# Kernel optimization log

Hardware: AMD Instinct MI355X
Metric: run time of the kernel (lower is better)

## Reference

```python
import jax, jax.numpy as jnp
import numpy as np

B = 128          # graphs
N = 512          # nodes per graph
NT = B * N       # total nodes = 65536
E = NT * 16      # total edges = 1048576
IN = 64
H = 128
OUT = 2
L = 4            # num_layers
RATIO = 0.8


def setup_inputs() -> dict:
    key = jax.random.key(0)
    ks = jax.random.split(key, 20)

    def w(k, shape, fan_in):
        return jax.random.normal(k, shape, jnp.float32) / np.sqrt(fan_in)

    x = jax.random.normal(ks[0], (NT, IN), jnp.float32)
    edge_index = jax.random.randint(ks[1], (2, E), 0, NT, dtype=jnp.int32)
    batch = (jnp.arange(NT) // N).astype(jnp.int32)  # equal-size graphs

    return {
        "x": x,
        "edge_index": edge_index,
        "batch": batch,
        # conv1: GraphConv(IN, H, aggr='mean') -> lin_rel (w/ bias) + lin_root (no bias)
        "W1_rel": w(ks[2], (IN, H), IN),
        "W1_root": w(ks[3], (IN, H), IN),
        "b1": jnp.zeros((H,), jnp.float32),
        # convs[0..2]: GraphConv(H, H, aggr='mean'), stacked
        "Wc_rel": w(ks[4], (L - 1, H, H), H),
        "Wc_root": w(ks[5], (L - 1, H, H), H),
        "bc": jnp.zeros((L - 1, H), jnp.float32),
        # SAGPooling score GNN: GraphConv(H, 1) with default aggr='add'
        "pw_rel": w(ks[6], (H,), H),
        "pw_root": w(ks[7], (H,), H),
        "pb": jnp.zeros((1,), jnp.float32),
        # MLP head
        "lin1_W": w(ks[8], (L * H, H), L * H),
        "lin1_b": jnp.zeros((H,), jnp.float32),
        "lin2_W": w(ks[9], (H, OUT), H),
        "lin2_b": jnp.zeros((OUT,), jnp.float32),
    }


def _graph_conv_mean(x, src, dst, emask, W_rel, W_root, b, n):
    # PyG GraphConv: lin_rel(mean_{j->i} x_j) + lin_root(x_i); masked edges excluded.
    msg = x[src] * emask[:, None]                                  # [E, D] gather
    s = jax.ops.segment_sum(msg, dst, num_segments=n)              # [n, D] scatter-add
    cnt = jax.ops.segment_sum(emask, dst, num_segments=n)          # [n]
    agg = s / jnp.maximum(cnt, 1.0)[:, None]                       # zero for isolated nodes
    return agg @ W_rel + x @ W_root + b


def reference(x, edge_index, batch, W1_rel, W1_root, b1, Wc_rel, Wc_root, bc,
              pw_rel, pw_root, pb, lin1_W, lin1_b, lin2_W, lin2_b):
    src = edge_index[0]
    dst = edge_index[1]
    emask = jnp.ones((E,), jnp.float32)
    n = NT
    npg = N  # nodes per graph (all graphs equal size)

    h = jax.nn.relu(_graph_conv_mean(x, src, dst, emask, W1_rel, W1_root, b1, n))
    xs = [h.reshape(B, npg, H).mean(axis=1)]  # global_mean_pool

    for i in range(L - 1):
        h = jax.nn.relu(_graph_conv_mean(h, src, dst, emask, Wc_rel[i], Wc_root[i], bc[i], n))
        xs.append(h.reshape(B, npg, H).mean(axis=1))
        if i % 2 == 0 and i < L - 2:
            # ---- SAGPooling: score via GraphConv(H,1) with add aggregation ----
            smsg = jax.ops.segment_sum(h[src] * emask[:, None], dst, num_segments=n)
            score = smsg @ pw_rel + h @ pw_root + pb[0]            # [n]
            k = int(np.ceil(RATIO * npg))
            topv, topi = jax.lax.top_k(score.reshape(B, npg), k)   # per-graph top-k
            perm = (jnp.arange(B)[:, None] * npg + topi).reshape(-1)  # global kept ids
            h = h[perm] * jnp.tanh(topv.reshape(-1))[:, None]
            # remap edges; edges touching dropped nodes get masked out
            node_map = jnp.full((n,), -1, jnp.int32).at[perm].set(
                jnp.arange(B * k, dtype=jnp.int32))
            ns, nd = node_map[src], node_map[dst]
            keep = ((ns >= 0) & (nd >= 0)).astype(jnp.float32)
            emask = emask * keep
            src = jnp.where(ns >= 0, ns, 0)
            dst = jnp.where(nd >= 0, nd, 0)
            n = B * k
            npg = k

    xcat = jnp.concatenate(xs, axis=-1)                            # JumpingKnowledge 'cat'
    out = jax.nn.relu(xcat @ lin1_W + lin1_b)
    # dropout is identity in eval mode
    out = out @ lin2_W + lin2_b
    return jax.nn.log_softmax(out, axis=-1)
```

## Files before the change

kernel.cpp:

```cpp
#include <hip/hip_runtime.h>
#include <math.h>

#define NT 65536
#define EE 1048576
#define NB 128
#define KK 410
#define HH 128

typedef short bf16x8 __attribute__((ext_vector_type(8)));
typedef float f32x4 __attribute__((ext_vector_type(4)));
typedef unsigned int u32x4 __attribute__((ext_vector_type(4)));

__device__ __align__(16) unsigned short g_xb[(size_t)NT * 64];
__device__ __align__(16) unsigned short g_hb1[(size_t)NT * HH];
__device__ __align__(16) unsigned short g_hb2[(size_t)NT * HH];
__device__ __align__(16) unsigned short g_wt1[128 * 128];
__device__ __align__(16) unsigned short g_wtc[3 * 128 * 256];
__device__ __align__(16) unsigned short g_xbs[(size_t)8 * NT * 8];
__device__ __align__(16) unsigned short g_hbs[(size_t)8 * NT * 16];
__device__ __align__(16) unsigned short g_agg[(size_t)16 * NT * 8];
__device__ unsigned short g_csr1u[EE];
__device__ unsigned short g_keptu[NT];
__device__ unsigned int g_ebuck[EE];
__device__ int g_bcnt[128];
__device__ int g_bbase[129];
__device__ int g_bcur[128];
__device__ float g_trel[NT];
__device__ float g_troot[NT];
__device__ float g_gatef[NT];
__device__ float g_kinv[NT];
__device__ float g_xc4[4 * NB * 4 * 128];
__device__ int g_rows1[NT + 1];

__device__ __forceinline__ unsigned short* ubuf(int id) {
    switch (id) {
        case 0: return g_xb;
        case 1: return g_hb1;
        case 2: return g_hb2;
        case 3: return g_wt1;
        case 4: return g_wtc;
    }
    return g_xb;
}

__device__ __forceinline__ float b2f(unsigned short u) {
    union { unsigned int i; float f; } v;
    v.i = ((unsigned int)u) << 16;
    return v.f;
}
__device__ __forceinline__ unsigned short f2b(float f) {
    unsigned int x = __float_as_uint(f);
    unsigned int r = x + 0x7fffu + ((x >> 16) & 1u);
    return (unsigned short)(r >> 16);
}
__device__ __forceinline__ unsigned int pk2(float a, float b) {
    return (unsigned int)f2b(a) | ((unsigned int)f2b(b) << 16);
}
__device__ __forceinline__ unsigned int mul2(unsigned int wd, float g) {
    float lo = b2f((unsigned short)(wd & 0xffffu)) * g;
    float hi = b2f((unsigned short)(wd >> 16)) * g;
    return pk2(lo, hi);
}
__device__ __forceinline__ bf16x8 scale8(bf16x8 a, float g) {
    bf16x8 r;
#pragma unroll
    for (int i = 0; i < 8; i++) {
        unsigned short u = (unsigned short)a[i];
        r[i] = (short)f2b(b2f(u) * g);
    }
    return r;
}

__global__ void k_prep(const float* __restrict__ x,
                       const float* __restrict__ W1r, const float* __restrict__ W1o,
                       const float* __restrict__ Wcr, const float* __restrict__ Wco) {
    int tid = blockIdx.x * 256 + threadIdx.x;
    if (tid < 1048576) {
        float4 v = *(const float4*)&x[(size_t)tid * 4];
        unsigned int lo = pk2(v.x, v.y);
        unsigned int hi = pk2(v.z, v.w);
        *(uint2*)&g_xb[(size_t)tid * 4] = make_uint2(lo, hi);
        int node = tid >> 4;
        int sl = (tid & 15) >> 1;
        int of = (tid & 1) * 4;
        *(uint2*)&g_xbs[(((size_t)sl) * NT + node) * 8 + of] = make_uint2(lo, hi);
    } else if (tid < 1048576 + 16384) {
        int r = tid - 1048576;
        int k = r & 127, n = r >> 7;
        float v = (k < 64) ? W1r[k * 128 + n] : W1o[(k - 64) * 128 + n];
        g_wt1[n * 128 + k] = f2b(v);
    } else if (tid < 1048576 + 16384 + 98304) {
        int r = tid - (1048576 + 16384);
        int l = r >> 15;
        int k = r & 255, n = (r >> 8) & 127;
        float v = (k < 128) ? Wcr[l * 16384 + k * 128 + n]
                            : Wco[l * 16384 + (k - 128) * 128 + n];
        g_wtc[l * 32768 + n * 256 + k] = f2b(v);
    } else if (tid < 1048576 + 16384 + 98304 + 128) {
        g_bcnt[tid - (1048576 + 16384 + 98304)] = 0;
    }
}

__global__ __launch_bounds__(256) void k_bhist(const int* __restrict__ dst) {
    __shared__ int h[128];
    if (threadIdx.x < 128) h[threadIdx.x] = 0;
    __syncthreads();
    int e0 = (blockIdx.x * 256 + threadIdx.x) * 4;
    int4 d = *(const int4*)&dst[e0];
    atomicAdd(&h[d.x >> 9], 1);
    atomicAdd(&h[d.y >> 9], 1);
    atomicAdd(&h[d.z >> 9], 1);
    atomicAdd(&h[d.w >> 9], 1);
    __syncthreads();
    if (threadIdx.x < 128 && h[threadIdx.x]) atomicAdd(&g_bcnt[threadIdx.x], h[threadIdx.x]);
}

__global__ __launch_bounds__(128) void k_bscan() {
    __shared__ int s[128];
    int t = threadIdx.x;
    int v = g_bcnt[t];
    s[t] = v;
    __syncthreads();
    for (int off = 1; off < 128; off <<= 1) {
        int u = (t >= off) ? s[t - off] : 0;
        __syncthreads();
        s[t] += u;
        __syncthreads();
    }
    g_bbase[t] = s[t] - v;
    g_bcur[t] = s[t] - v;
    if (t == 127) g_bbase[128] = s[127];
}

__global__ __launch_bounds__(256) void k_bscatter(const int* __restrict__ src,
// ... 14 lines not shown
    if (threadIdx.x < 128) {
        int c = h[threadIdx.x];
        base[threadIdx.x] = c ? atomicAdd(&g_bcur[threadIdx.x], c) : 0;
        h[threadIdx.x] = 0;
    }
    __syncthreads();
    int r0 = atomicAdd(&h[b0], 1);
    g_ebuck[base[b0] + r0] = ((unsigned int)(d.x & 511) << 16) | (unsigned int)s.x;
    int r1 = atomicAdd(&h[b1], 1);
    g_ebuck[base[b1] + r1] = ((unsigned int)(d.y & 511) << 16) | (unsigned int)s.y;
    int r2 = atomicAdd(&h[b2], 1);
    g_ebuck[base[b2] + r2] = ((unsigned int)(d.z & 511) << 16) | (unsigned int)s.z;
    int r3 = atomicAdd(&h[b3], 1);
    g_ebuck[base[b3] + r3] = ((unsigned int)(d.w & 511) << 16) | (unsigned int)s.w;
}

__global__ __launch_bounds__(512) void k_bcsr() {
    __shared__ int hist[512];
    __shared__ int offs[512];
    __shared__ int cur[512];
    int g = blockIdx.x, t = threadIdx.x;
    hist[t] = 0;
    cur[t] = 0;
    __syncthreads();
    int b0 = g_bbase[g], b1 = g_bbase[g + 1];
    for (int e = b0 + t; e < b1; e += 512) {
        unsigned int p = g_ebuck[e];
        atomicAdd(&hist[p >> 16], 1);
    }
    __syncthreads();
    int v = hist[t];
    offs[t] = v;
    __syncthreads();
    for (int off = 1; off < 512; off <<= 1) {
        int u = (t >= off) ? offs[t - off] : 0;
        __syncthreads();
        offs[t] += u;
        __syncthreads();
    }
    int excl = offs[t] - v;
    g_rows1[g * 512 + t] = b0 + excl;
    if (t == 511) g_rows1[g * 512 + 512] = b0 + excl + v;
    __syncthreads();
    offs[t] = excl;
    __syncthreads();
    for (int e = b0 + t; e < b1; e += 512) {
        unsigned int p = g_ebuck[e];
        int dl = p >> 16;
        int r = atomicAdd(&cur[dl], 1);
        g_csr1u[b0 + offs[dl] + r] = (unsigned short)(p & 0xFFFFu);
    }
}

#define ACCP(wd, J) { acc[J] += b2f((unsigned short)((wd) & 0xffffu)); acc[(J) + 1] += b2f((unsigned short)((wd) >> 16)); }
#define ACCQ(q, B) ACCP(q.x, B) ACCP(q.y, (B) + 2) ACCP(q.z, (B) + 4) ACCP(q.w, (B) + 6)

template <int F, int DEN>
__global__ __launch_bounds__(256) void k_agg(int srcId) {
    const unsigned short* src = (srcId == 0) ? g_xbs : g_hbs;
    int s = blockIdx.x & 7;
    int node = (blockIdx.x >> 3) * 256 + threadIdx.x;
    const unsigned short* sp = src + (size_t)s * NT * F;
    int r0 = g_rows1[node], r1 = g_rows1[node + 1];
    float inv;
    if (DEN) {
        inv = g_kinv[node];
    } else {
        int c = r1 - r0;
        inv = 1.0f / (float)(c > 0 ? c : 1);
    }
    float acc[F];
#pragma unroll
    for (int i = 0; i < F; i++) acc[i] = 0.f;
    int e = r0;
    for (; e + 2 <= r1; e += 2) {
        int i0 = g_csr1u[e], i1 = g_csr1u[e + 1];
        if constexpr (F == 16) {
            uint4 a0 = *(const uint4*)&sp[(size_t)i0 * 16];
            uint4 a1 = *(const uint4*)&sp[(size_t)i0 * 16 + 8];
            uint4 b0 = *(const uint4*)&sp[(size_t)i1 * 16];
            uint4 b1 = *(const uint4*)&sp[(size_t)i1 * 16 + 8];
            ACCQ(a0, 0) ACCQ(a1, 8) ACCQ(b0, 0) ACCQ(b1, 8)
        } else {
            uint4 a0 = *(const uint4*)&sp[(size_t)i0 * 8];
            uint4 b0 = *(const uint4*)&sp[(size_t)i1 * 8];
            ACCQ(a0, 0) ACCQ(b0, 0)
        }
    }
    for (; e < r1; e++) {
        int i0 = g_csr1u[e];
        if constexpr (F == 16) {
            uint4 a0 = *(const uint4*)&sp[(size_t)i0 * 16];
            uint4 a1 = *(const uint4*)&sp[(size_t)i0 * 16 + 8];
            ACCQ(a0, 0) ACCQ(a1, 8)
        } else {
            uint4 a0 = *(const uint4*)&sp[(size_t)i0 * 8];
            ACCQ(a0, 0)
        }
    }
    int gb = (F == 16) ? (2 * s) : s;
    u32x4 o;
    o[0] = pk2(acc[0] * inv, acc[1] * inv);
    o[1] = pk2(acc[2] * inv, acc[3] * inv);
    o[2] = pk2(acc[4] * inv, acc[5] * inv);
    o[3] = pk2(acc[6] * inv, acc[7] * inv);
    __builtin_nontemporal_store(o, (u32x4*)&g_agg[((size_t)gb * NT + node) * 8]);
    if constexpr (F == 16) {
        u32x4 o2;
        o2[0] = pk2(acc[8] * inv, acc[9] * inv);
        o2[1] = pk2(acc[10] * inv, acc[11] * inv);
        o2[2] = pk2(acc[12] * inv, acc[13] * inv);
        o2[3] = pk2(acc[14] * inv, acc[15] * inv);
        __builtin_nontemporal_store(o2, (u32x4*)&g_agg[((size_t)(2 * s + 1) * NT + node) * 8]);
    }
}

__global__ __launch_bounds__(256) void k_kinv() {
    int node = blockIdx.x * 256 + threadIdx.x;
    int r0 = g_rows1[node], r1 = g_rows1[node + 1];
    int kc = 0;
    for (int e = r0; e < r1; e++) kc += (int)g_keptu[g_csr1u[e]];
    g_kinv[node] = 1.0f / (float)(kc > 0 ? kc : 1);
}

__global__ __launch_bounds__(256) void k_gateS() {
    int tid = blockIdx.x * 256 + threadIdx.x;
    int n = tid >> 3, s = tid & 7;
    float g = g_gatef[n];
    const unsigned short* srcp = &g_hb2[(size_t)n * 128 + s * 16];
    uint4 a = *(const uint4*)srcp;
    uint4 b = *(const uint4*)(srcp + 8);
    uint4 oa, ob;
    oa.x = mul2(a.x, g); oa.y = mul2(a.y, g); oa.z = mul2(a.z, g); oa.w = mul2(a.w, g);
    ob.x = mul2(b.x, g); ob.y = mul2(b.y, g); ob.z = mul2(b.z, g); ob.w = mul2(b.w, g);
    unsigned short* d = &g_hbs[((size_t)s * NT + n) * 16];
    *(uint4*)d = oa;
    *(uint4*)(d + 8) = ob;
}

template <int KA, int KB, int MASKED, int DOTS, int BGATE, int WSL>
__global__ __launch_bounds__(256) void k_mm(int bId, int wId, int wOfs,
                                            const float* __restrict__ bias, int outId, int sec,
                                            const float* __restrict__ pwr,
                                            const float* __restrict__ pwt) {
    __shared__ float s[128];
    const unsigned short* Bp = ubuf(bId);
    const unsigned short* Wt = ubuf(wId) + wOfs;
    unsigned short* out = ubuf(outId);
    int rowbase = blockIdx.x * 128;
    const int K = KA + KB;
    int lane = threadIdx.x & 63;
    int w = threadIdx.x >> 6;
    int n16 = lane & 15, quad = lane >> 4;
    int rowloc = w * 32;
    int rowg = rowbase + rowloc;
    int g = blockIdx.x >> 2, qb = blockIdx.x & 3;
    float ga0 = BGATE ? g_gatef[rowg + n16] : 1.0f;
    float ga1 = BGATE ? g_gatef[rowg + 16 + n16] : 1.0f;
    f32x4 acc[2][8];
#pragma unroll
    for (int rt = 0; rt < 2; rt++)
#pragma unroll
        for (int ct = 0; ct < 8; ct++)
#pragma unroll
            for (int i = 0; i < 4; i++) acc[rt][ct][i] = 0.f;

#pragma unroll
    for (int ks = 0; ks < K / 32; ks++) {
        int k0 = ks * 32;
        bf16x8 a0, a1;
        if (k0 < KA) {
            int fg = (k0 + quad * 8) >> 3;
            a0 = *(const bf16x8*)&g_agg[((size_t)fg * NT + rowg + n16) * 8];
            a1 = *(const bf16x8*)&g_agg[((size_t)fg * NT + rowg + 16 + n16) * 8];
        } else {
            int kk = k0 - KA;
            a0 = *(const bf16x8*)&Bp[(size_t)(rowg + n16) * KB + kk + quad * 8];
            a1 = *(const bf16x8*)&Bp[(size_t)(rowg + 16 + n16) * KB + kk + quad * 8];
            if (BGATE) { a0 = scale8(a0, ga0); a1 = scale8(a1, ga1); }
        }
#pragma unroll
        for (int ct = 0; ct < 8; ct++) {
            bf16x8 b = *(const bf16x8*)&Wt[(size_t)(ct * 16 + n16) * K + k0 + quad * 8];
            acc[0][ct] = __builtin_amdgcn_mfma_f32_16x16x32_bf16(a0, b, acc[0][ct], 0, 0, 0);
            acc[1][ct] = __builtin_amdgcn_mfma_f32_16x16x32_bf16(a1, b, acc[1][ct], 0, 0, 0);
        }
    }

    if (threadIdx.x < 128) s[threadIdx.x] = 0.f;
#pragma unroll
    for (int rt = 0; rt < 2; rt++) {
        float m[4];
#pragma unroll
        for (int i = 0; i < 4; i++) {
            int r = rowg + rt * 16 + quad * 4 + i;
            m[i] = (!MASKED || g_keptu[r]) ? 1.0f : 0.0f;
        }
#pragma unroll
        for (int ct = 0; ct < 8; ct++) {
            int c = ct * 16 + n16;
            float bv = bias[c];
#pragma unroll
            for (int i = 0; i < 4; i++) {
                int r = rowg + rt * 16 + quad * 4 + i;
                float v = fmaxf(acc[rt][ct][i] + bv, 0.f) * m[i];
                acc[rt][ct][i] = v;
                unsigned short hv = f2b(v);
                out[(size_t)r * 128 + c] = hv;
                if (WSL) g_hbs[((size_t)(c >> 4) * NT + r) * 16 + (c & 15)] = hv;
            }
        }
    }
    __syncthreads();

#pragma unroll
    for (int ct = 0; ct < 8; ct++) {
        float p = 0.f;
#pragma unroll
        for (int rt = 0; rt < 2; rt++)
#pragma unroll
            for (int i = 0; i < 4; i++) p += acc[rt][ct][i];
        p += __shfl_xor(p, 16);
        p += __shfl_xor(p, 32);
        if (quad == 0) atomicAdd(&s[ct * 16 + n16], p);
    }

    if (DOTS) {
        float pr[8], pt[8];
#pragma unroll
        for (int ct = 0; ct < 8; ct++) {
            pr[ct] = pwr[ct * 16 + n16];
            pt[ct] = pwt[ct * 16 + n16];
        }
#pragma unroll
        for (int rt = 0; rt < 2; rt++)
#pragma unroll
            for (int i = 0; i < 4; i++) {
                float dr = 0.f, dt = 0.f;
#pragma unroll
                for (int ct = 0; ct < 8; ct++) {
                    dr += acc[rt][ct][i] * pr[ct];
                    dt += acc[rt][ct][i] * pt[ct];
                }
                dr += __shfl_xor(dr, 1); dt += __shfl_xor(dt, 1);
                dr += __shfl_xor(dr, 2); dt += __shfl_xor(dt, 2);
                dr += __shfl_xor(dr, 4); dt += __shfl_xor(dt, 4);
                dr += __shfl_xor(dr, 8); dt += __shfl_xor(dt, 8);
                if (n16 == 0) {
                    int r = rowg + rt * 16 + quad * 4 + i;
                    g_trel[r] = dr;
                    g_troot[r] = dt;
                }
            }
    }
    __syncthreads();
    if (threadIdx.x < 128)
        g_xc4[((sec * NB + g) * 4 + qb) * 128 + threadIdx.x] = s[threadIdx.x];
}

__global__ __launch_bounds__(256) void k_topk(const float* __restrict__ pb) {
    __shared__ float sv[512];
    __shared__ int si[512];
    int g = blockIdx.x, t = threadIdx.x;
    float pbv = pb[0];
    for (int l = t; l < 512; l += 256) {
        int node = g * 512 + l;
        int r0 = g_rows1[node], r1 = g_rows1[node + 1];
        float s = 0.f;
        int e = r0;
        for (; e + 4 <= r1; e += 4) {
            float s0 = g_trel[g_csr1u[e]];
            float s1 = g_trel[g_csr1u[e + 1]];
            float s2 = g_trel[g_csr1u[e + 2]];
            float s3 = g_trel[g_csr1u[e + 3]];
            s += (s0 + s1) + (s2 + s3);
        }
        for (; e < r1; e++) s += g_trel[g_csr1u[e]];
        sv[l] = s + g_troot[node] + pbv;
        si[l] = l;
    }
    __syncthreads();
    for (int k = 2; k <= 512; k <<= 1) {
        for (int j = k >> 1; j > 0; j >>= 1) {
            for (int i = t; i < 512; i += 256) {
                int p = i ^ j;
                if (p > i) {
                    float va = sv[i], vb = sv[p];
                    int ia = si[i], ib = si[p];
                    bool aFirst = (va > vb) || (va == vb && ia < ib);
                    bool up = ((i & k) == 0);
                    if (up != aFirst) { sv[i] = vb; sv[p] = va; si[i] = ib; si[p] = ia; }
                }
            }
            __syncthreads();
        }
    }
    for (int r = t; r < 512; r += 256) {
        int old = g * 512 + si[r];
        if (r < KK) {
            g_gatef[old] = tanhf(sv[r]);
            g_keptu[old] = 1;
        } else {
            g_gatef[old] = 0.f;
            g_keptu[old] = 0;
        }
    }
}

__global__ __launch_bounds__(128) void k_head(const float* __restrict__ W1, const float* __restrict__ b1,
                                              const float* __restrict__ W2, const float* __restrict__ b2,
// ... 6 lines not shown
        const float* p = &g_xc4[((sec * NB + g) * 4) * 128 + c];
        float v = p[0] + p[128] + p[256] + p[384];
        float inv = (sec < 2) ? (1.0f / 512.0f) : (1.0f / 410.0f);
        xr[i] = v * inv;
    }
    __syncthreads();
    float acc = b1[t];
    for (int k = 0; k < 512; k++) acc += xr[k] * W1[k * 128 + t];
    acc = fmaxf(acc, 0.f);
    r0[t] = acc * W2[t * 2 + 0];
    r1[t] = acc * W2[t * 2 + 1];
    __syncthreads();
    for (int off = 64; off > 0; off >>= 1) {
        if (t < off) { r0[t] += r0[t + off]; r1[t] += r1[t + off]; }
        __syncthreads();
    }
    if (t == 0) {
        float z0 = r0[0] + b2[0], z1 = r1[0] + b2[1];
        float m = fmaxf(z0, z1);
        float l = m + logf(expf(z0 - m) + expf(z1 - m));
        out[g * 2 + 0] = z0 - l;
        out[g * 2 + 1] = z1 - l;
    }
}

extern "C" void kernel_launch(void* const* d_in, const int* in_sizes, int n_in,
                              void* d_out, int out_size, void* d_ws, size_t ws_size,
                              hipStream_t stream) {
    const float* x = (const float*)d_in[0];
    const int* ei = (const int*)d_in[1];
    const int* src = ei;
    const int* dst = ei + EE;
    const float* W1r = (const float*)d_in[3];
    const float* W1o = (const float*)d_in[4];
    const float* b1 = (const float*)d_in[5];
    const float* Wcr = (const float*)d_in[6];
    const float* Wco = (const float*)d_in[7];
    const float* bc = (const float*)d_in[8];
    const float* pwr = (const float*)d_in[9];
    const float* pwt = (const float*)d_in[10];
    const float* pb = (const float*)d_in[11];
    const float* l1W = (const float*)d_in[12];
    const float* l1b = (const float*)d_in[13];
    const float* l2W = (const float*)d_in[14];
    const float* l2b = (const float*)d_in[15];
    float* out = (float*)d_out;

    k_prep<<<(1048576 + 16384 + 98304 + 128 + 255) / 256, 256, 0, stream>>>(x, W1r, W1o, Wcr, Wco);

    k_bhist<<<1024, 256, 0, stream>>>(dst);
    k_bscan<<<1, 128, 0, stream>>>();
    k_bscatter<<<1024, 256, 0, stream>>>(src, dst);
    k_bcsr<<<128, 512, 0, stream>>>();

    k_agg<8, 0><<<2048, 256, 0, stream>>>(0);
    k_mm<64, 64, 0, 0, 0, 1><<<512, 256, 0, stream>>>(0, 3, 0, b1, 1, 0, pwr, pwt);

    k_agg<16, 0><<<2048, 256, 0, stream>>>(1);
    k_mm<128, 128, 0, 1, 0, 0><<<512, 256, 0, stream>>>(1, 4, 0, bc, 2, 1, pwr, pwt);

    k_topk<<<NB, 256, 0, stream>>>(pb);
    k_kinv<<<NT / 256, 256, 0, stream>>>();
    k_gateS<<<2048, 256, 0, stream>>>();

    k_agg<16, 1><<<2048, 256, 0, stream>>>(1);
    k_mm<128, 128, 1, 0, 1, 1><<<512, 256, 0, stream>>>(2, 4, 32768, bc + 128, 1, 2, pwr, pwt);

    k_agg<16, 1><<<2048, 256, 0, stream>>>(1);
    k_mm<128, 128, 1, 0, 0, 0><<<512, 256, 0, stream>>>(1, 4, 65536, bc + 256, 2, 3, pwr, pwt);

    k_head<<<NB, 128, 0, stream>>>(l1W, l1b, l2W, l2b, out);
}
```

Measured before the change: 529.3 us.

## Degree-sort aggregation nodes, store activations sliced, gather last layer in 8-bit

Adds a per-graph node permutation sorted by in-degree so each aggregation wavefront processes nodes of similar edge counts, which reduces loop divergence. CSR neighbour indices are now read four at a time. Layer activations are written only in the feature-sliced layout through a shared-memory transpose, and the matmul root operand reads that layout, which removes the extra row-major copy. The last layer's neighbour gather reads a custom 8-bit float encoding (values clamped at 496) instead of bf16, halving the gather bytes at the cost of extra precision loss.

```diff
diff --git a/kernel.cpp b/kernel.cpp
--- a/kernel.cpp
+++ b/kernel.cpp
@@ -11,20 +11,21 @@
 typedef float f32x4 __attribute__((ext_vector_type(4)));
 typedef unsigned int u32x4 __attribute__((ext_vector_type(4)));
 
-__device__ __align__(16) unsigned short g_xb[(size_t)NT * 64];
-__device__ __align__(16) unsigned short g_hb1[(size_t)NT * HH];
+__device__ __align__(16) unsigned short g_xbs[(size_t)8 * NT * 8];
+__device__ __align__(16) unsigned short g_hs1[(size_t)8 * NT * 16];
+__device__ __align__(16) unsigned short g_hgs[(size_t)8 * NT * 16];
 __device__ __align__(16) unsigned short g_hb2[(size_t)NT * HH];
+__device__ __align__(16) unsigned char  g_h8b[(size_t)8 * NT * 16];
+__device__ __align__(16) unsigned short g_agg[(size_t)16 * NT * 8];
 __device__ __align__(16) unsigned short g_wt1[128 * 128];
 __device__ __align__(16) unsigned short g_wtc[3 * 128 * 256];
-__device__ __align__(16) unsigned short g_xbs[(size_t)8 * NT * 8];
-__device__ __align__(16) unsigned short g_hbs[(size_t)8 * NT * 16];
-__device__ __align__(16) unsigned short g_agg[(size_t)16 * NT * 8];
-__device__ unsigned short g_csr1u[EE];
+__device__ __align__(16) unsigned short g_csr1u[EE];
 __device__ unsigned short g_keptu[NT];
 __device__ unsigned int g_ebuck[EE];
 __device__ int g_bcnt[128];
 __device__ int g_bbase[129];
 __device__ int g_bcur[128];
+__device__ int g_nperm[NT];
 __device__ float g_trel[NT];
 __device__ float g_troot[NT];
 __device__ float g_gatef[NT];
@@ -32,16 +33,7 @@
 __device__ float g_xc4[4 * NB * 4 * 128];
 __device__ int g_rows1[NT + 1];
 
-__device__ __forceinline__ unsigned short* ubuf(int id) {
-    switch (id) {
-        case 0: return g_xb;
-        case 1: return g_hb1;
-        case 2: return g_hb2;
-        case 3: return g_wt1;
-        case 4: return g_wtc;
-    }
-    return g_xb;
-}
+__device__ __forceinline__ unsigned short* wbuf(int id) { return id ? g_wtc : g_wt1; }
 
 __device__ __forceinline__ float b2f(unsigned short u) {
     union { unsigned int i; float f; } v;
@@ -61,15 +53,13 @@
     float hi = b2f((unsigned short)(wd >> 16)) * g;
     return pk2(lo, hi);
 }
-__device__ __forceinline__ bf16x8 scale8(bf16x8 a, float g) {
-    bf16x8 r;
-#pragma unroll
-    for (int i = 0; i < 8; i++) {
-        unsigned short u = (unsigned short)a[i];
-        r[i] = (short)f2b(b2f(u) * g);
-    }
-    return r;
-}
+__device__ __forceinline__ unsigned char enc8(float v) {
+    v = fminf(v, 496.0f);
+    unsigned int b = __float_as_uint(v * 0x1p-120f);
+    unsigned int r = (b + 0x3ffffu + ((b >> 19) & 1u)) >> 19;
+    return (unsigned char)r;
+}
+#define DEC8(u) ((u) ? __uint_as_float(((unsigned int)(u) << 19) + 0x3C000000u) : 0.0f)
 
 __global__ void k_prep(const float* __restrict__ x,
                        const float* __restrict__ W1r, const float* __restrict__ W1o,
@@ -79,7 +69,6 @@
         float4 v = *(const float4*)&x[(size_t)tid * 4];
         unsigned int lo = pk2(v.x, v.y);
         unsigned int hi = pk2(v.z, v.w);
-        *(uint2*)&g_xb[(size_t)tid * 4] = make_uint2(lo, hi);
         int node = tid >> 4;
         int sl = (tid & 15) >> 1;
         int of = (tid & 1) * 4;
@@ -200,15 +189,42 @@
     }
 }
 
+__global__ __launch_bounds__(512) void k_dperm() {
+    __shared__ int h[64];
+    __shared__ int base[64];
+    int g = blockIdx.x, t = threadIdx.x;
+    if (t < 64) h[t] = 0;
+    __syncthreads();
+    int n = g * 512 + t;
+    int d = min(g_rows1[n + 1] - g_rows1[n], 63);
+    atomicAdd(&h[d], 1);
+    __syncthreads();
+    if (t == 0) {
+        int ss = 0;
+        for (int i = 0; i < 64; i++) { base[i] = ss; ss += h[i]; }
+    }
+    __syncthreads();
+    int pos = atomicAdd(&base[d], 1);
+    g_nperm[g * 512 + pos] = n;
+}
+
 #define ACCP(wd, J) { acc[J] += b2f((unsigned short)((wd) & 0xffffu)); acc[(J) + 1] += b2f((unsigned short)((wd) >> 16)); }
 #define ACCQ(q, B) ACCP(q.x, B) ACCP(q.y, (B) + 2) ACCP(q.z, (B) + 4) ACCP(q.w, (B) + 6)
 
-template <int F, int DEN>
+template <int F, int DEN, int FP8>
 __global__ __launch_bounds__(256) void k_agg(int srcId) {
-    const unsigned short* src = (srcId == 0) ? g_xbs : g_hbs;
     int s = blockIdx.x & 7;
-    int node = (blockIdx.x >> 3) * 256 + threadIdx.x;
-    const unsigned short* sp = src + (size_t)s * NT * F;
+    int idx = (blockIdx.x >> 3) * 256 + threadIdx.x;
+    int node = g_nperm[idx];
+    const unsigned short* sp = nullptr;
+    const unsigned char* sp8 = nullptr;
+    if constexpr (FP8) {
+        sp8 = g_h8b + (size_t)s * NT * 16;
+    } else if constexpr (F == 8) {
+        sp = g_xbs + (size_t)s * NT * 8;
+    } else {
+        sp = (srcId == 0 ? g_hs1 : g_hgs) + (size_t)s * NT * 16;
+    }
     int r0 = g_rows1[node], r1 = g_rows1[node + 1];
     float inv;
     if (DEN) {
@@ -217,49 +233,65 @@
         int c = r1 - r0;
         inv = 1.0f / (float)(c > 0 ? c : 1);
     }
-    float acc[F];
-#pragma unroll
-    for (int i = 0; i < F; i++) acc[i] = 0.f;
+    constexpr int NA = FP8 ? 16 : F;
+    float acc[NA];
+#pragma unroll
+    for (int i = 0; i < NA; i++) acc[i] = 0.f;
+
+    auto body = [&](int ii) {
+        if constexpr (FP8) {
+            uint4 w = *(const uint4*)&sp8[(size_t)ii * 16];
+            acc[0] += DEC8(w.x & 0xffu);
+            acc[1] += DEC8((w.x >> 8) & 0xffu);
+            acc[2] += DEC8((w.x >> 16) & 0xffu);
+            acc[3] += DEC8(w.x >> 24);
+            acc[4] += DEC8(w.y & 0xffu);
+            acc[5] += DEC8((w.y >> 8) & 0xffu);
+            acc[6] += DEC8((w.y >> 16) & 0xffu);
+            acc[7] += DEC8(w.y >> 24);
+            acc[8] += DEC8(w.z & 0xffu);
+            acc[9] += DEC8((w.z >> 8) & 0xffu);
+            acc[10] += DEC8((w.z >> 16) & 0xffu);
+            acc[11] += DEC8(w.z >> 24);
+            acc[12] += DEC8(w.w & 0xffu);
+            acc[13] += DEC8((w.w >> 8) & 0xffu);
+            acc[14] += DEC8((w.w >> 16) & 0xffu);
+            acc[15] += DEC8(w.w >> 24);
+        } else if constexpr (F == 8) {
+            uint4 v = *(const uint4*)&sp[(size_t)ii * 8];
+            ACCQ(v, 0)
+        } else {
+            uint4 v = *(const uint4*)&sp[(size_t)ii * 16];
+            uint4 v2 = *(const uint4*)&sp[(size_t)ii * 16 + 8];
+            ACCQ(v, 0) ACCQ(v2, 8)
+        }
+    };
+
     int e = r0;
-    for (; e + 2 <= r1; e += 2) {
-        int i0 = g_csr1u[e], i1 = g_csr1u[e + 1];
-        if constexpr (F == 16) {
-            uint4 a0 = *(const uint4*)&sp[(size_t)i0 * 16];
-            uint4 a1 = *(const uint4*)&sp[(size_t)i0 * 16 + 8];
-            uint4 b0 = *(const uint4*)&sp[(size_t)i1 * 16];
-            uint4 b1 = *(const uint4*)&sp[(size_t)i1 * 16 + 8];
-            ACCQ(a0, 0) ACCQ(a1, 8) ACCQ(b0, 0) ACCQ(b1, 8)
-        } else {
-            uint4 a0 = *(const uint4*)&sp[(size_t)i0 * 8];
-            uint4 b0 = *(const uint4*)&sp[(size_t)i1 * 8];
-            ACCQ(a0, 0) ACCQ(b0, 0)
-        }
-    }
-    for (; e < r1; e++) {
-        int i0 = g_csr1u[e];
-        if constexpr (F == 16) {
-            uint4 a0 = *(const uint4*)&sp[(size_t)i0 * 16];
-            uint4 a1 = *(const uint4*)&sp[(size_t)i0 * 16 + 8];
-            ACCQ(a0, 0) ACCQ(a1, 8)
-        } else {
-            uint4 a0 = *(const uint4*)&sp[(size_t)i0 * 8];
-            ACCQ(a0, 0)
-        }
-    }
-    int gb = (F == 16) ? (2 * s) : s;
+    for (; e < r1 && (e & 3); e++) body((int)g_csr1u[e]);
+    for (; e + 4 <= r1; e += 4) {
+        uint2 iv = *(const uint2*)&g_csr1u[e];
+        body((int)(iv.x & 0xffffu));
+        body((int)(iv.x >> 16));
+        body((int)(iv.y & 0xffffu));
+        body((int)(iv.y >> 16));
+    }
+    for (; e < r1; e++) body((int)g_csr1u[e]);
+
+    int gb0 = (NA == 8) ? s : 2 * s;
     u32x4 o;
     o[0] = pk2(acc[0] * inv, acc[1] * inv);
     o[1] = pk2(acc[2] * inv, acc[3] * inv);
     o[2] = pk2(acc[4] * inv, acc[5] * inv);
     o[3] = pk2(acc[6] * inv, acc[7] * inv);
-    __builtin_nontemporal_store(o, (u32x4*)&g_agg[((size_t)gb * NT + node) * 8]);
-    if constexpr (F == 16) {
+    __builtin_nontemporal_store(o, (u32x4*)&g_agg[((size_t)gb0 * NT + node) * 8]);
+    if constexpr (NA == 16) {
         u32x4 o2;
         o2[0] = pk2(acc[8] * inv, acc[9] * inv);
         o2[1] = pk2(acc[10] * inv, acc[11] * inv);
         o2[2] = pk2(acc[12] * inv, acc[13] * inv);
         o2[3] = pk2(acc[14] * inv, acc[15] * inv);
-        __builtin_nontemporal_store(o2, (u32x4*)&g_agg[((size_t)(2 * s + 1) * NT + node) * 8]);
+        __builtin_nontemporal_store(o2, (u32x4*)&g_agg[((size_t)(gb0 + 1) * NT + node) * 8]);
     }
 }
 
@@ -267,7 +299,14 @@
     int node = blockIdx.x * 256 + threadIdx.x;
     int r0 = g_rows1[node], r1 = g_rows1[node + 1];
     int kc = 0;
-    for (int e = r0; e < r1; e++) kc += (int)g_keptu[g_csr1u[e]];
+    int e = r0;
+    for (; e < r1 && (e & 3); e++) kc += (int)g_keptu[g_csr1u[e]];
+    for (; e + 4 <= r1; e += 4) {
+        uint2 iv = *(const uint2*)&g_csr1u[e];
+        kc += (int)g_keptu[iv.x & 0xffffu] + (int)g_keptu[iv.x >> 16]
+            + (int)g_keptu[iv.y & 0xffffu] + (int)g_keptu[iv.y >> 16];
+    }
+    for (; e < r1; e++) kc += (int)g_keptu[g_csr1u[e]];
     g_kinv[node] = 1.0f / (float)(kc > 0 ? kc : 1);
 }
 
@@ -281,20 +320,21 @@
     uint4 oa, ob;
     oa.x = mul2(a.x, g); oa.y = mul2(a.y, g); oa.z = mul2(a.z, g); oa.w = mul2(a.w, g);
     ob.x = mul2(b.x, g); ob.y = mul2(b.y, g); ob.z = mul2(b.z, g); ob.w = mul2(b.w, g);
-    unsigned short* d = &g_hbs[((size_t)s * NT + n) * 16];
+    unsigned short* d = &g_hgs[((size_t)s * NT + n) * 16];
     *(uint4*)d = oa;
     *(uint4*)(d + 8) = ob;
 }
 
-template <int KA, int KB, int MASKED, int DOTS, int BGATE, int WSL>
-__global__ __launch_bounds__(256) void k_mm(int bId, int wId, int wOfs,
-                                            const float* __restrict__ bias, int outId, int sec,
+template <int KA, int KB, int MASKED, int DOTS, int ROOTK, int OUTK>
+__global__ __launch_bounds__(256) void k_mm(int wsel, int wOfs,
+                                            int rootSel,
+                                            const float* __restrict__ bias, int sec,
                                             const float* __restrict__ pwr,
                                             const float* __restrict__ pwt) {
     __shared__ float s[128];
-    const unsigned short* Bp = ubuf(bId);
-    const unsigned short* Wt = ubuf(wId) + wOfs;
-    unsigned short* out = ubuf(outId);
+    __shared__ unsigned short t16[(OUTK >= 2) ? 128 * 136 : 2];
+    const unsigned short* Wt = wbuf(wsel) + wOfs;
+    const unsigned short* sb = (ROOTK == 1) ? (rootSel ? g_hgs : g_hs1) : g_xbs;
     int rowbase = blockIdx.x * 128;
     const int K = KA + KB;
     int lane = threadIdx.x & 63;
@@ -303,8 +343,6 @@
     int rowloc = w * 32;
     int rowg = rowbase + rowloc;
     int g = blockIdx.x >> 2, qb = blockIdx.x & 3;
-    float ga0 = BGATE ? g_gatef[rowg + n16] : 1.0f;
-    float ga1 = BGATE ? g_gatef[rowg + 16 + n16] : 1.0f;
     f32x4 acc[2][8];
 #pragma unroll
     for (int rt = 0; rt < 2; rt++)
@@ -322,10 +360,16 @@
             a0 = *(const bf16x8*)&g_agg[((size_t)fg * NT + rowg + n16) * 8];
             a1 = *(const bf16x8*)&g_agg[((size_t)fg * NT + rowg + 16 + n16) * 8];
         } else {
-            int kk = k0 - KA;
-            a0 = *(const bf16x8*)&Bp[(size_t)(rowg + n16) * KB + kk + quad * 8];
-            a1 = *(const bf16x8*)&Bp[(size_t)(rowg + 16 + n16) * KB + kk + quad * 8];
-            if (BGATE) { a0 = scale8(a0, ga0); a1 = scale8(a1, ga1); }
+            int col = k0 - KA + quad * 8;
+            if constexpr (ROOTK == 0) {
+                int fg = col >> 3;
+                a0 = *(const bf16x8*)&g_xbs[((size_t)fg * NT + rowg + n16) * 8];
+                a1 = *(const bf16x8*)&g_xbs[((size_t)fg * NT + rowg + 16 + n16) * 8];
+            } else {
+                int fg = col >> 4, off = col & 15;
+                a0 = *(const bf16x8*)&sb[((size_t)fg * NT + rowg + n16) * 16 + off];
+                a1 = *(const bf16x8*)&sb[((size_t)fg * NT + rowg + 16 + n16) * 16 + off];
+            }
         }
 #pragma unroll
         for (int ct = 0; ct < 8; ct++) {
@@ -353,9 +397,8 @@
                 int r = rowg + rt * 16 + quad * 4 + i;
                 float v = fmaxf(acc[rt][ct][i] + bv, 0.f) * m[i];
                 acc[rt][ct][i] = v;
-                unsigned short hv = f2b(v);
-                out[(size_t)r * 128 + c] = hv;
-                if (WSL) g_hbs[((size_t)(c >> 4) * NT + r) * 16 + (c & 15)] = hv;
+                if constexpr (OUTK == 1) g_hb2[(size_t)r * 128 + c] = f2b(v);
+                if constexpr (OUTK >= 2) t16[(rowloc + rt * 16 + quad * 4 + i) * 136 + c] = f2b(v);
             }
         }
     }
@@ -404,6 +447,37 @@
     __syncthreads();
     if (threadIdx.x < 128)
         g_xc4[((sec * NB + g) * 4 + qb) * 128 + threadIdx.x] = s[threadIdx.x];
+
+    if constexpr (OUTK >= 2) {
+        int tid = threadIdx.x;
+#pragma unroll
+        for (int rep = 0; rep < 8; rep++) {
+            int chunk = rep * 256 + tid;
+            int s_ = chunk >> 8, rem = chunk & 255;
+            int nl = rem >> 1, hf = rem & 1;
+            bf16x8 val = *(const bf16x8*)&t16[nl * 136 + s_ * 16 + hf * 8];
+            *(bf16x8*)&g_hs1[((size_t)s_ * NT + rowbase + nl) * 16 + hf * 8] = val;
+        }
+        if constexpr (OUTK == 3) {
+#pragma unroll
+            for (int rep = 0; rep < 4; rep++) {
+                int chunk = rep * 256 + tid;
+                int s_ = chunk >> 7, nl = chunk & 127;
+                const unsigned short* p = &t16[nl * 136 + s_ * 16];
+                unsigned int wq[4];
+#pragma unroll
+                for (int q = 0; q < 4; q++) {
+                    unsigned int c0 = enc8(b2f(p[q * 4 + 0]));
+                    unsigned int c1 = enc8(b2f(p[q * 4 + 1]));
+                    unsigned int c2 = enc8(b2f(p[q * 4 + 2]));
+                    unsigned int c3 = enc8(b2f(p[q * 4 + 3]));
+                    wq[q] = c0 | (c1 << 8) | (c2 << 16) | (c3 << 24);
+                }
+                *(uint4*)&g_h8b[((size_t)s_ * NT + rowbase + nl) * 16] =
+                    make_uint4(wq[0], wq[1], wq[2], wq[3]);
+            }
+        }
+    }
 }
 
 __global__ __launch_bounds__(256) void k_topk(const float* __restrict__ pb) {
@@ -516,22 +590,23 @@
     k_bscan<<<1, 128, 0, stream>>>();
     k_bscatter<<<1024, 256, 0, stream>>>(src, dst);
     k_bcsr<<<128, 512, 0, stream>>>();
-
-    k_agg<8, 0><<<2048, 256, 0, stream>>>(0);
-    k_mm<64, 64, 0, 0, 0, 1><<<512, 256, 0, stream>>>(0, 3, 0, b1, 1, 0, pwr, pwt);
-
-    k_agg<16, 0><<<2048, 256, 0, stream>>>(1);
-    k_mm<128, 128, 0, 1, 0, 0><<<512, 256, 0, stream>>>(1, 4, 0, bc, 2, 1, pwr, pwt);
+    k_dperm<<<NB, 512, 0, stream>>>();
+
+    k_agg<8, 0, 0><<<2048, 256, 0, stream>>>(0);
+    k_mm<64, 64, 0, 0, 0, 2><<<512, 256, 0, stream>>>(0, 0, 0, b1, 0, pwr, pwt);
+
+    k_agg<16, 0, 0><<<2048, 256, 0, stream>>>(0);
+    k_mm<128, 128, 0, 1, 1, 1><<<512, 256, 0, stream>>>(1, 0, 0, bc, 1, pwr, pwt);
 
     k_topk<<<NB, 256, 0, stream>>>(pb);
     k_kinv<<<NT / 256, 256, 0, stream>>>();
     k_gateS<<<2048, 256, 0, stream>>>();
 
-    k_agg<16, 1><<<2048, 256, 0, stream>>>(1);
-    k_mm<128, 128, 1, 0, 1, 1><<<512, 256, 0, stream>>>(2, 4, 32768, bc + 128, 1, 2, pwr, pwt);
-
-    k_agg<16, 1><<<2048, 256, 0, stream>>>(1);
-    k_mm<128, 128, 1, 0, 0, 0><<<512, 256, 0, stream>>>(1, 4, 65536, bc + 256, 2, 3, pwr, pwt);
+    k_agg<16, 1, 0><<<2048, 256, 0, stream>>>(1);
+    k_mm<128, 128, 1, 0, 1, 3><<<512, 256, 0, stream>>>(1, 32768, 1, bc + 128, 2, pwr, pwt);
+
+    k_agg<16, 1, 1><<<2048, 256, 0, stream>>>(0);
+    k_mm<128, 128, 1, 0, 1, 0><<<512, 256, 0, stream>>>(1, 65536, 0, bc + 256, 3, pwr, pwt);
 
     k_head<<<NB, 128, 0, stream>>>(l1W, l1b, l2W, l2b, out);
 }
```

Result: no change. 531.1 us (+0.3%).

## Fuse neighbor aggregation into GEMM kernel via LDS-staged aggregated rows

Applied to the files above, without the earlier changes.

Replaces the separate aggregation and matmul kernels with one fused conv kernel. Each 512-thread block aggregates neighbor features for its 128 rows into LDS, sorting rows by degree for load balance, then runs the MFMA GEMM reading the aggregate from LDS and root features from sliced global buffers. This drops the global round trip of the aggregated buffer and several launches. Layer outputs are now written in sliced layout from LDS and CSR indices are read four at a time. The cost is less parallelism in the gather, since there are fewer blocks and each thread walks 8 slices serially, plus higher LDS use per block.

```diff
diff --git a/kernel.cpp b/kernel.cpp
--- a/kernel.cpp
+++ b/kernel.cpp
@@ -9,17 +9,14 @@
 
 typedef short bf16x8 __attribute__((ext_vector_type(8)));
 typedef float f32x4 __attribute__((ext_vector_type(4)));
-typedef unsigned int u32x4 __attribute__((ext_vector_type(4)));
-
-__device__ __align__(16) unsigned short g_xb[(size_t)NT * 64];
-__device__ __align__(16) unsigned short g_hb1[(size_t)NT * HH];
+
+__device__ __align__(16) unsigned short g_xbs[(size_t)8 * NT * 8];
+__device__ __align__(16) unsigned short g_hs1[(size_t)8 * NT * 16];
+__device__ __align__(16) unsigned short g_hgs[(size_t)8 * NT * 16];
 __device__ __align__(16) unsigned short g_hb2[(size_t)NT * HH];
 __device__ __align__(16) unsigned short g_wt1[128 * 128];
 __device__ __align__(16) unsigned short g_wtc[3 * 128 * 256];
-__device__ __align__(16) unsigned short g_xbs[(size_t)8 * NT * 8];
-__device__ __align__(16) unsigned short g_hbs[(size_t)8 * NT * 16];
-__device__ __align__(16) unsigned short g_agg[(size_t)16 * NT * 8];
-__device__ unsigned short g_csr1u[EE];
+__device__ __align__(16) unsigned short g_csr1u[EE];
 __device__ unsigned short g_keptu[NT];
 __device__ unsigned int g_ebuck[EE];
 __device__ int g_bcnt[128];
@@ -32,17 +29,6 @@
 __device__ float g_xc4[4 * NB * 4 * 128];
 __device__ int g_rows1[NT + 1];
 
-__device__ __forceinline__ unsigned short* ubuf(int id) {
-    switch (id) {
-        case 0: return g_xb;
-        case 1: return g_hb1;
-        case 2: return g_hb2;
-        case 3: return g_wt1;
-        case 4: return g_wtc;
-    }
-    return g_xb;
-}
-
 __device__ __forceinline__ float b2f(unsigned short u) {
     union { unsigned int i; float f; } v;
     v.i = ((unsigned int)u) << 16;
@@ -61,14 +47,9 @@
     float hi = b2f((unsigned short)(wd >> 16)) * g;
     return pk2(lo, hi);
 }
-__device__ __forceinline__ bf16x8 scale8(bf16x8 a, float g) {
-    bf16x8 r;
-#pragma unroll
-    for (int i = 0; i < 8; i++) {
-        unsigned short u = (unsigned short)a[i];
-        r[i] = (short)f2b(b2f(u) * g);
-    }
-    return r;
+__device__ __forceinline__ void acc2(float* a, unsigned int wd) {
+    a[0] += b2f((unsigned short)(wd & 0xffffu));
+    a[1] += b2f((unsigned short)(wd >> 16));
 }
 
 __global__ void k_prep(const float* __restrict__ x,
@@ -79,7 +60,6 @@
         float4 v = *(const float4*)&x[(size_t)tid * 4];
         unsigned int lo = pk2(v.x, v.y);
         unsigned int hi = pk2(v.z, v.w);
-        *(uint2*)&g_xb[(size_t)tid * 4] = make_uint2(lo, hi);
         int node = tid >> 4;
         int sl = (tid & 15) >> 1;
         int of = (tid & 1) * 4;
@@ -200,66 +180,206 @@
     }
 }
 
-#define ACCP(wd, J) { acc[J] += b2f((unsigned short)((wd) & 0xffffu)); acc[(J) + 1] += b2f((unsigned short)((wd) >> 16)); }
-#define ACCQ(q, B) ACCP(q.x, B) ACCP(q.y, (B) + 2) ACCP(q.z, (B) + 4) ACCP(q.w, (B) + 6)
-
-template <int F, int DEN>
-__global__ __launch_bounds__(256) void k_agg(int srcId) {
-    const unsigned short* src = (srcId == 0) ? g_xbs : g_hbs;
-    int s = blockIdx.x & 7;
-    int node = (blockIdx.x >> 3) * 256 + threadIdx.x;
-    const unsigned short* sp = src + (size_t)s * NT * F;
-    int r0 = g_rows1[node], r1 = g_rows1[node + 1];
-    float inv;
-    if (DEN) {
-        inv = g_kinv[node];
-    } else {
-        int c = r1 - r0;
-        inv = 1.0f / (float)(c > 0 ? c : 1);
-    }
-    float acc[F];
-#pragma unroll
-    for (int i = 0; i < F; i++) acc[i] = 0.f;
-    int e = r0;
-    for (; e + 2 <= r1; e += 2) {
-        int i0 = g_csr1u[e], i1 = g_csr1u[e + 1];
-        if constexpr (F == 16) {
-            uint4 a0 = *(const uint4*)&sp[(size_t)i0 * 16];
-            uint4 a1 = *(const uint4*)&sp[(size_t)i0 * 16 + 8];
-            uint4 b0 = *(const uint4*)&sp[(size_t)i1 * 16];
-            uint4 b1 = *(const uint4*)&sp[(size_t)i1 * 16 + 8];
-            ACCQ(a0, 0) ACCQ(a1, 8) ACCQ(b0, 0) ACCQ(b1, 8)
+template <int KA, int DEN, int MASKED, int DOTS, int OUTK>
+__global__ __launch_bounds__(512, 4) void k_conv(int sbufId, int wsel, int wOfs,
+                                                 const float* __restrict__ bias, int sec,
+                                                 const float* __restrict__ pwr,
+                                                 const float* __restrict__ pwt) {
+    constexpr int F = (KA == 64) ? 8 : 16;
+    constexpr int FQ = F / 4;
+    constexpr int STRA = KA + 8;
+    __shared__ unsigned short lds_a[128 * 136];
+    __shared__ float s[128];
+    __shared__ unsigned short sord[128];
+    __shared__ int dh[64];
+    __shared__ int db[64];
+    const unsigned short* sb =
+        (KA == 64) ? g_xbs : ((sbufId == 2) ? g_hgs : g_hs1);
+    const unsigned short* Wt = (wsel ? g_wtc : g_wt1) + wOfs;
+    int rowbase = blockIdx.x * 128;
+
+    if (threadIdx.x < 64) dh[threadIdx.x] = 0;
+    __syncthreads();
+    if (threadIdx.x < 128) {
+        int node = rowbase + threadIdx.x;
+        int d = min(g_rows1[node + 1] - g_rows1[node], 63);
+        atomicAdd(&dh[d], 1);
+    }
+    __syncthreads();
+    if (threadIdx.x == 0) {
+        int ss = 0;
+        for (int i = 0; i < 64; i++) { db[i] = ss; ss += dh[i]; }
+    }
+    __syncthreads();
+    if (threadIdx.x < 128) {
+        int node = rowbase + threadIdx.x;
+        int d = min(g_rows1[node + 1] - g_rows1[node], 63);
+        int p = atomicAdd(&db[d], 1);
+        sord[p] = (unsigned short)threadIdx.x;
+    }
+    __syncthreads();
+
+    {
+        int row = sord[threadIdx.x >> 2];
+        int q = threadIdx.x & 3;
+        int node = rowbase + row;
+        int r0 = g_rows1[node], r1 = g_rows1[node + 1];
+        float inv;
+        if (DEN) {
+            inv = g_kinv[node];
         } else {
-            uint4 a0 = *(const uint4*)&sp[(size_t)i0 * 8];
-            uint4 b0 = *(const uint4*)&sp[(size_t)i1 * 8];
-            ACCQ(a0, 0) ACCQ(b0, 0)
-        }
-    }
-    for (; e < r1; e++) {
-        int i0 = g_csr1u[e];
-        if constexpr (F == 16) {
-            uint4 a0 = *(const uint4*)&sp[(size_t)i0 * 16];
-            uint4 a1 = *(const uint4*)&sp[(size_t)i0 * 16 + 8];
-            ACCQ(a0, 0) ACCQ(a1, 8)
+            int c = r1 - r0;
+            inv = 1.0f / (float)(c > 0 ? c : 1);
+        }
+#pragma unroll 1
+        for (int sl = 0; sl < 8; sl++) {
+            const unsigned short* sp = sb + ((size_t)sl * NT) * F + q * FQ;
+            float acc[FQ];
+#pragma unroll
+            for (int i = 0; i < FQ; i++) acc[i] = 0.f;
+
+#define BODY(ii) {                                                   \
+    if constexpr (FQ == 4) {                                         \
+        uint2 v = *(const uint2*)&sp[(size_t)(ii) * 16];             \
+        acc2(acc, v.x); acc2(acc + 2, v.y);                          \
+    } else {                                                         \
+        unsigned int v = *(const unsigned int*)&sp[(size_t)(ii) * 8];\
+        acc2(acc, v);                                                \
+    }                                                                \
+}
+            int e = r0;
+            for (; e < r1 && (e & 3); e++) BODY((int)g_csr1u[e]);
+            for (; e + 4 <= r1; e += 4) {
+                uint2 iv = *(const uint2*)&g_csr1u[e];
+                BODY((int)(iv.x & 0xffffu));
+                BODY((int)(iv.x >> 16));
+                BODY((int)(iv.y & 0xffffu));
+                BODY((int)(iv.y >> 16));
+            }
+            for (; e < r1; e++) BODY((int)g_csr1u[e]);
+#undef BODY
+            if constexpr (FQ == 4) {
+                *(uint2*)&lds_a[row * STRA + sl * F + q * 4] =
+                    make_uint2(pk2(acc[0] * inv, acc[1] * inv),
+                               pk2(acc[2] * inv, acc[3] * inv));
+            } else {
+                *(unsigned int*)&lds_a[row * STRA + sl * F + q * 2] =
+                    pk2(acc[0] * inv, acc[1] * inv);
+            }
+        }
+    }
+    if (threadIdx.x < 128) s[threadIdx.x] = 0.f;
+    __syncthreads();
+
+    const int K = 2 * KA;
+    int lane = threadIdx.x & 63;
+    int w = threadIdx.x >> 6;
+    int n16 = lane & 15, quad = lane >> 4;
+    int rowloc = w * 16;
+    int rowg = rowbase + rowloc;
+    int g = blockIdx.x >> 2, qb = blockIdx.x & 3;
+    f32x4 acc[8];
+#pragma unroll
+    for (int ct = 0; ct < 8; ct++)
+#pragma unroll
+        for (int i = 0; i < 4; i++) acc[ct][i] = 0.f;
+
+#pragma unroll
+    for (int ks = 0; ks < K / 32; ks++) {
+        int k0 = ks * 32;
+        bf16x8 a0;
+        if (k0 < KA) {
+            a0 = *(const bf16x8*)&lds_a[(rowloc + n16) * STRA + k0 + quad * 8];
         } else {
-            uint4 a0 = *(const uint4*)&sp[(size_t)i0 * 8];
-            ACCQ(a0, 0)
-        }
-    }
-    int gb = (F == 16) ? (2 * s) : s;
-    u32x4 o;
-    o[0] = pk2(acc[0] * inv, acc[1] * inv);
-    o[1] = pk2(acc[2] * inv, acc[3] * inv);
-    o[2] = pk2(acc[4] * inv, acc[5] * inv);
-    o[3] = pk2(acc[6] * inv, acc[7] * inv);
-    __builtin_nontemporal_store(o, (u32x4*)&g_agg[((size_t)gb * NT + node) * 8]);
-    if constexpr (F == 16) {
-        u32x4 o2;
-        o2[0] = pk2(acc[8] * inv, acc[9] * inv);
-        o2[1] = pk2(acc[10] * inv, acc[11] * inv);
-        o2[2] = pk2(acc[12] * inv, acc[13] * inv);
-        o2[3] = pk2(acc[14] * inv, acc[15] * inv);
-        __builtin_nontemporal_store(o2, (u32x4*)&g_agg[((size_t)(2 * s + 1) * NT + node) * 8]);
+            int col = k0 - KA + quad * 8;
+            if constexpr (KA == 64) {
+                int fg = col >> 3;
+                a0 = *(const bf16x8*)&sb[((size_t)fg * NT + rowg + n16) * 8];
+            } else {
+                int fg = col >> 4, off = col & 15;
+                a0 = *(const bf16x8*)&sb[((size_t)fg * NT + rowg + n16) * 16 + off];
+            }
+        }
+#pragma unroll
+        for (int ct = 0; ct < 8; ct++) {
+            bf16x8 b = *(const bf16x8*)&Wt[(size_t)(ct * 16 + n16) * K + k0 + quad * 8];
+            acc[ct] = __builtin_amdgcn_mfma_f32_16x16x32_bf16(a0, b, acc[ct], 0, 0, 0);
+        }
+    }
+    __syncthreads();
+
+    {
+        float m[4];
+#pragma unroll
+        for (int i = 0; i < 4; i++) {
+            int r = rowg + quad * 4 + i;
+            m[i] = (!MASKED || g_keptu[r]) ? 1.0f : 0.0f;
+        }
+#pragma unroll
+        for (int ct = 0; ct < 8; ct++) {
+            int c = ct * 16 + n16;
+            float bv = bias[c];
+#pragma unroll
+            for (int i = 0; i < 4; i++) {
+                float v = fmaxf(acc[ct][i] + bv, 0.f) * m[i];
+                acc[ct][i] = v;
+                if constexpr (OUTK == 1)
+                    g_hb2[(size_t)(rowg + quad * 4 + i) * 128 + c] = f2b(v);
+                if constexpr (OUTK == 2)
+                    lds_a[(rowloc + quad * 4 + i) * 136 + c] = f2b(v);
+            }
+        }
+    }
+
+#pragma unroll
+    for (int ct = 0; ct < 8; ct++) {
+        float p = 0.f;
+#pragma unroll
+        for (int i = 0; i < 4; i++) p += acc[ct][i];
+        p += __shfl_xor(p, 16);
+        p += __shfl_xor(p, 32);
+        if (quad == 0) atomicAdd(&s[ct * 16 + n16], p);
+    }
+
+    if (DOTS) {
+        float pr[8], pt[8];
+#pragma unroll
+        for (int ct = 0; ct < 8; ct++) {
+            pr[ct] = pwr[ct * 16 + n16];
+            pt[ct] = pwt[ct * 16 + n16];
+        }
+#pragma unroll
+        for (int i = 0; i < 4; i++) {
+            float dr = 0.f, dt = 0.f;
+#pragma unroll
+            for (int ct = 0; ct < 8; ct++) {
+                dr += acc[ct][i] * pr[ct];
+                dt += acc[ct][i] * pt[ct];
+            }
+            dr += __shfl_xor(dr, 1); dt += __shfl_xor(dt, 1);
+            dr += __shfl_xor(dr, 2); dt += __shfl_xor(dt, 2);
+            dr += __shfl_xor(dr, 4); dt += __shfl_xor(dt, 4);
+            dr += __shfl_xor(dr, 8); dt += __shfl_xor(dt, 8);
+            if (n16 == 0) {
+                int r = rowg + quad * 4 + i;
+                g_trel[r] = dr;
+                g_troot[r] = dt;
+            }
+        }
+    }
+    __syncthreads();
+    if (threadIdx.x < 128)
+        g_xc4[((sec * NB + g) * 4 + qb) * 128 + threadIdx.x] = s[threadIdx.x];
+
+    if constexpr (OUTK == 2) {
+#pragma unroll
+        for (int rep = 0; rep < 4; rep++) {
+            int chunk = rep * 512 + threadIdx.x;
+            int s_ = chunk >> 8, rem = chunk & 255;
+            int nl = rem >> 1, hf = rem & 1;
+            bf16x8 val = *(const bf16x8*)&lds_a[nl * 136 + s_ * 16 + hf * 8];
+            *(bf16x8*)&g_hs1[((size_t)s_ * NT + rowbase + nl) * 16 + hf * 8] = val;
+        }
     }
 }
 
@@ -267,7 +387,14 @@
     int node = blockIdx.x * 256 + threadIdx.x;
     int r0 = g_rows1[node], r1 = g_rows1[node + 1];
     int kc = 0;
-    for (int e = r0; e < r1; e++) kc += (int)g_keptu[g_csr1u[e]];
+    int e = r0;
+    for (; e < r1 && (e & 3); e++) kc += (int)g_keptu[g_csr1u[e]];
+    for (; e + 4 <= r1; e += 4) {
+        uint2 iv = *(const uint2*)&g_csr1u[e];
+        kc += (int)g_keptu[iv.x & 0xffffu] + (int)g_keptu[iv.x >> 16]
+            + (int)g_keptu[iv.y & 0xffffu] + (int)g_keptu[iv.y >> 16];
+    }
+    for (; e < r1; e++) kc += (int)g_keptu[g_csr1u[e]];
     g_kinv[node] = 1.0f / (float)(kc > 0 ? kc : 1);
 }
 
@@ -281,129 +408,9 @@
     uint4 oa, ob;
     oa.x = mul2(a.x, g); oa.y = mul2(a.y, g); oa.z = mul2(a.z, g); oa.w = mul2(a.w, g);
     ob.x = mul2(b.x, g); ob.y = mul2(b.y, g); ob.z = mul2(b.z, g); ob.w = mul2(b.w, g);
-    unsigned short* d = &g_hbs[((size_t)s * NT + n) * 16];
+    unsigned short* d = &g_hgs[((size_t)s * NT + n) * 16];
     *(uint4*)d = oa;
     *(uint4*)(d + 8) = ob;
-}
-
-template <int KA, int KB, int MASKED, int DOTS, int BGATE, int WSL>
-__global__ __launch_bounds__(256) void k_mm(int bId, int wId, int wOfs,
-                                            const float* __restrict__ bias, int outId, int sec,
-                                            const float* __restrict__ pwr,
-                                            const float* __restrict__ pwt) {
-    __shared__ float s[128];
-    const unsigned short* Bp = ubuf(bId);
-    const unsigned short* Wt = ubuf(wId) + wOfs;
-    unsigned short* out = ubuf(outId);
-    int rowbase = blockIdx.x * 128;
-    const int K = KA + KB;
-    int lane = threadIdx.x & 63;
-    int w = threadIdx.x >> 6;
-    int n16 = lane & 15, quad = lane >> 4;
-    int rowloc = w * 32;
-    int rowg = rowbase + rowloc;
-    int g = blockIdx.x >> 2, qb = blockIdx.x & 3;
-    float ga0 = BGATE ? g_gatef[rowg + n16] : 1.0f;
-    float ga1 = BGATE ? g_gatef[rowg + 16 + n16] : 1.0f;
-    f32x4 acc[2][8];
-#pragma unroll
-    for (int rt = 0; rt < 2; rt++)
-#pragma unroll
-        for (int ct = 0; ct < 8; ct++)
-#pragma unroll
-            for (int i = 0; i < 4; i++) acc[rt][ct][i] = 0.f;
-
-#pragma unroll
-    for (int ks = 0; ks < K / 32; ks++) {
-        int k0 = ks * 32;
-        bf16x8 a0, a1;
-        if (k0 < KA) {
-            int fg = (k0 + quad * 8) >> 3;
-            a0 = *(const bf16x8*)&g_agg[((size_t)fg * NT + rowg + n16) * 8];
-            a1 = *(const bf16x8*)&g_agg[((size_t)fg * NT + rowg + 16 + n16) * 8];
-        } else {
-            int kk = k0 - KA;
-            a0 = *(const bf16x8*)&Bp[(size_t)(rowg + n16) * KB + kk + quad * 8];
-            a1 = *(const bf16x8*)&Bp[(size_t)(rowg + 16 + n16) * KB + kk + quad * 8];
-            if (BGATE) { a0 = scale8(a0, ga0); a1 = scale8(a1, ga1); }
-        }
-#pragma unroll
-        for (int ct = 0; ct < 8; ct++) {
-            bf16x8 b = *(const bf16x8*)&Wt[(size_t)(ct * 16 + n16) * K + k0 + quad * 8];
-            acc[0][ct] = __builtin_amdgcn_mfma_f32_16x16x32_bf16(a0, b, acc[0][ct], 0, 0, 0);
-            acc[1][ct] = __builtin_amdgcn_mfma_f32_16x16x32_bf16(a1, b, acc[1][ct], 0, 0, 0);
-        }
-    }
-
-    if (threadIdx.x < 128) s[threadIdx.x] = 0.f;
-#pragma unroll
-    for (int rt = 0; rt < 2; rt++) {
-        float m[4];
-#pragma unroll
-        for (int i = 0; i < 4; i++) {
-            int r = rowg + rt * 16 + quad * 4 + i;
-            m[i] = (!MASKED || g_keptu[r]) ? 1.0f : 0.0f;
-        }
-#pragma unroll
-        for (int ct = 0; ct < 8; ct++) {
-            int c = ct * 16 + n16;
-            float bv = bias[c];
-#pragma unroll
-            for (int i = 0; i < 4; i++) {
-                int r = rowg + rt * 16 + quad * 4 + i;
-                float v = fmaxf(acc[rt][ct][i] + bv, 0.f) * m[i];
-                acc[rt][ct][i] = v;
-                unsigned short hv = f2b(v);
-                out[(size_t)r * 128 + c] = hv;
-                if (WSL) g_hbs[((size_t)(c >> 4) * NT + r) * 16 + (c & 15)] = hv;
-            }
-        }
-    }
-    __syncthreads();
-
-#pragma unroll
-    for (int ct = 0; ct < 8; ct++) {
-        float p = 0.f;
-#pragma unroll
-        for (int rt = 0; rt < 2; rt++)
-#pragma unroll
-            for (int i = 0; i < 4; i++) p += acc[rt][ct][i];
-        p += __shfl_xor(p, 16);
-        p += __shfl_xor(p, 32);
-        if (quad == 0) atomicAdd(&s[ct * 16 + n16], p);
-    }
-
-    if (DOTS) {
-        float pr[8], pt[8];
-#pragma unroll
-        for (int ct = 0; ct < 8; ct++) {
-            pr[ct] = pwr[ct * 16 + n16];
-            pt[ct] = pwt[ct * 16 + n16];
-        }
-#pragma unroll
-        for (int rt = 0; rt < 2; rt++)
-#pragma unroll
-            for (int i = 0; i < 4; i++) {
-                float dr = 0.f, dt = 0.f;
-#pragma unroll
-                for (int ct = 0; ct < 8; ct++) {
-                    dr += acc[rt][ct][i] * pr[ct];
-                    dt += acc[rt][ct][i] * pt[ct];
-                }
-                dr += __shfl_xor(dr, 1); dt += __shfl_xor(dt, 1);
-                dr += __shfl_xor(dr, 2); dt += __shfl_xor(dt, 2);
-                dr += __shfl_xor(dr, 4); dt += __shfl_xor(dt, 4);
-                dr += __shfl_xor(dr, 8); dt += __shfl_xor(dt, 8);
-                if (n16 == 0) {
-                    int r = rowg + rt * 16 + quad * 4 + i;
-                    g_trel[r] = dr;
-                    g_troot[r] = dt;
-                }
-            }
-    }
-    __syncthreads();
-    if (threadIdx.x < 128)
-        g_xc4[((sec * NB + g) * 4 + qb) * 128 + threadIdx.x] = s[threadIdx.x];
 }
 
 __global__ __launch_bounds__(256) void k_topk(const float* __restrict__ pb) {
@@ -517,21 +524,17 @@
     k_bscatter<<<1024, 256, 0, stream>>>(src, dst);
     k_bcsr<<<128, 512, 0, stream>>>();
 
-    k_agg<8, 0><<<2048, 256, 0, stream>>>(0);
-    k_mm<64, 64, 0, 0, 0, 1><<<512, 256, 0, stream>>>(0, 3, 0, b1, 1, 0, pwr, pwt);
-
-    k_agg<16, 0><<<2048, 256, 0, stream>>>(1);
-    k_mm<128, 128, 0, 1, 0, 0><<<512, 256, 0, stream>>>(1, 4, 0, bc, 2, 1, pwr, pwt);
+    k_conv<64, 0, 0, 0, 2><<<512, 512, 0, stream>>>(0, 0, 0, b1, 0, pwr, pwt);
+
+    k_conv<128, 0, 0, 1, 1><<<512, 512, 0, stream>>>(1, 1, 0, bc, 1, pwr, pwt);
 
     k_topk<<<NB, 256, 0, stream>>>(pb);
     k_kinv<<<NT / 256, 256, 0, stream>>>();
     k_gateS<<<2048, 256, 0, stream>>>();
 
-    k_agg<16, 1><<<2048, 256, 0, stream>>>(1);
-    k_mm<128, 128, 1, 0, 1, 1><<<512, 256, 0, stream>>>(2, 4, 32768, bc + 128, 1, 2, pwr, pwt);
-
-    k_agg<16, 1><<<2048, 256, 0, stream>>>(1);
-    k_mm<128, 128, 1, 0, 0, 0><<<512, 256, 0, stream>>>(1, 4, 65536, bc + 256, 2, 3, pwr, pwt);
+    k_conv<128, 1, 1, 0, 2><<<512, 512, 0, stream>>>(2, 1, 32768, bc + 128, 2, pwr, pwt);
+
+    k_conv<128, 1, 1, 0, 0><<<512, 512, 0, stream>>>(1, 1, 65536, bc + 256, 3, pwr, pwt);
 
     k_head<<<NB, 128, 0, stream>>>(l1W, l1b, l2W, l2b, out);
 }
```

Result: slower. 630.0 us (+19.0%).
